# Kernel tuning notes

Hardware: AMD Instinct MI355X
Metric: run time of the kernel (lower is better)

Reference implementation:

```python
import jax, jax.numpy as jnp
import numpy as np

E, TWO_I, H = 8, 3072, 2048
I = TWO_I // 2
T = 16384

def setup_inputs() -> dict:
    key = jax.random.key(0)
    k1, k2, k3 = jax.random.split(key, 3)
    scale_gu = 1.0 / np.sqrt(H)
    scale_dn = 1.0 / np.sqrt(I)
    return {
        "current_state": jax.random.normal(k1, (T, H), dtype=jnp.float32),
        "gate_up_proj": jax.random.normal(k2, (E, TWO_I, H), dtype=jnp.float32) * scale_gu,
        "down_proj": jax.random.normal(k3, (E, H, I), dtype=jnp.float32) * scale_dn,
        "expert_idx": 3,
    }

def reference(current_state, gate_up_proj, down_proj, expert_idx):
    # F.linear(x, W) == x @ W.T
    w_gu = gate_up_proj[expert_idx]            # [2I, H]
    w_dn = down_proj[expert_idx]               # [H, I]
    gu = jnp.einsum("th,ih->ti", current_state, w_gu)  # [T, 2I]
    gate, up = jnp.split(gu, 2, axis=-1)       # each [T, I]
    hidden = jax.nn.silu(gate) * up            # SwiGLU gating
    return jnp.einsum("ti,hi->th", hidden, w_dn)  # [T, H]
```

## Files before the change

kernel.cpp:

```cpp
#include <hip/hip_runtime.h>
#include <hip/hip_bf16.h>


namespace {

constexpr int T_ = 16384;
constexpr int H_ = 2048;
constexpr int I_ = 1536;

typedef short short8 __attribute__((ext_vector_type(8)));
typedef float f32x4 __attribute__((ext_vector_type(4)));
typedef unsigned short ushort4v __attribute__((ext_vector_type(4)));

__device__ __forceinline__ unsigned short f2bf(float f) {
    union { float f; unsigned u; } v; v.f = f;
    return (unsigned short)((v.u + 0x7FFFu + ((v.u >> 16) & 1u)) >> 16);
}

typedef __attribute__((address_space(1))) const void gvoid;
typedef __attribute__((address_space(3))) void lvoid;
__device__ __forceinline__ void gload16(const void* g, void* l) {
    __builtin_amdgcn_global_load_lds((gvoid*)g, (lvoid*)l, 16, 0, 0);
}

__global__ void k_cvt(const float* __restrict__ base, const int* __restrict__ eidx,
                      long sliceElems, unsigned short* __restrict__ dst, int n4) {
    const float* src = base + (size_t)(*eidx) * (size_t)sliceElems;
    int i = blockIdx.x * blockDim.x + threadIdx.x;
    const int stride = gridDim.x * blockDim.x;
    for (; i < n4; i += stride) {
        f32x4 v = ((const f32x4*)src)[i];
        ushort4v h = { f2bf(v[0]), f2bf(v[1]), f2bf(v[2]), f2bf(v[3]) };
        ((ushort4v*)dst)[i] = h;
    }
}

__global__ __launch_bounds__(256, 2) void k_gemm1_swiglu(
    const unsigned short* __restrict__ xb, const unsigned short* __restrict__ wgub,
    unsigned short* __restrict__ hidden)
{
    __shared__ unsigned short lds[3 * 128 * 64];
    unsigned short* ldsA  = lds;
    unsigned short* ldsBg = lds + 128 * 64;
    unsigned short* ldsBu = lds + 2 * 128 * 64;

    const int tid  = threadIdx.x;
    const int lane = tid & 63;
    const int wv   = tid >> 6;
    const int wr   = wv >> 1, wc = wv & 1;

    const int nb = (blockIdx.x & 7) * 192 + (blockIdx.x >> 3);
    const int bx = nb % 12, by = nb / 12;
    const int m0 = by * 128;
    const int n0 = bx * 128;

    f32x4 accG[4][4], accU[4][4];
    #pragma unroll
    for (int a = 0; a < 4; ++a)
        #pragma unroll
        for (int b = 0; b < 4; ++b) { accG[a][b] = (f32x4)0.0f; accU[a][b] = (f32x4)0.0f; }

    const int drow = lane >> 3;
    const int dcol = (lane & 7) * 8;
    const int l15 = lane & 15;
    const int l4  = lane >> 4;

    for (int k0 = 0; k0 < H_; k0 += 64) {
        __syncthreads();
        #pragma unroll
        for (int r = 0; r < 4; ++r) {
            const int row  = r * 32 + wv * 8 + drow;
            const int loff = r * 2048 + wv * 512;
            gload16(xb   + (size_t)(m0 + row)      * H_ + k0 + dcol, ldsA  + loff);
            gload16(wgub + (size_t)(n0 + row)      * H_ + k0 + dcol, ldsBg + loff);
            gload16(wgub + (size_t)(I_ + n0 + row) * H_ + k0 + dcol, ldsBu + loff);
        }
        __syncthreads();

        #pragma unroll
        for (int kk = 0; kk < 2; ++kk) {
            short8 af[4], bg[4], bu[4];
            #pragma unroll
            for (int a = 0; a < 4; ++a) {
                const int r = wr * 64 + a * 16 + l15;
                af[a] = *(const short8*)(ldsA + r * 64 + kk * 32 + l4 * 8);
            }
            #pragma unroll
            for (int b = 0; b < 4; ++b) {
                const int r = wc * 64 + b * 16 + l15;
                bg[b] = *(const short8*)(ldsBg + r * 64 + kk * 32 + l4 * 8);
                bu[b] = *(const short8*)(ldsBu + r * 64 + kk * 32 + l4 * 8);
            }
            #pragma unroll
            for (int a = 0; a < 4; ++a)
                #pragma unroll
                for (int b = 0; b < 4; ++b) {
                    accG[a][b] = __builtin_amdgcn_mfma_f32_16x16x32_bf16(af[a], bg[b], accG[a][b], 0, 0, 0);
                    accU[a][b] = __builtin_amdgcn_mfma_f32_16x16x32_bf16(af[a], bu[b], accU[a][b], 0, 0, 0);
                }
        }
    }

    #pragma unroll
    for (int a = 0; a < 4; ++a)
        #pragma unroll
        for (int b = 0; b < 4; ++b)
            #pragma unroll
            for (int j = 0; j < 4; ++j) {
                const int row = m0 + wr * 64 + a * 16 + l4 * 4 + j;
                const int col = n0 + wc * 64 + b * 16 + l15;
                const float g = accG[a][b][j];
                const float u = accU[a][b][j];
                const float s = g / (1.0f + __expf(-g));
                hidden[(size_t)row * I_ + col] = f2bf(s * u);
            }
}

__global__ __launch_bounds__(256, 2) void k_gemm2(
    const unsigned short* __restrict__ hidden, const unsigned short* __restrict__ wdnb,
    float* __restrict__ out)
{
    __shared__ unsigned short lds[2 * 128 * 64];
    unsigned short* ldsA = lds;
    unsigned short* ldsB = lds + 128 * 64;

    const int tid  = threadIdx.x;
    const int lane = tid & 63;
    const int wv   = tid >> 6;
    const int wr   = wv >> 1, wc = wv & 1;

    const int nb = (blockIdx.x & 7) * 256 + (blockIdx.x >> 3);
    const int bx = nb % 16, by = nb / 16;
    const int m0 = by * 128;
    const int n0 = bx * 128;

    f32x4 acc[4][4];
    #pragma unroll
    for (int a = 0; a < 4; ++a)
        #pragma unroll
        for (int b = 0; b < 4; ++b) acc[a][b] = (f32x4)0.0f;

    const int drow = lane >> 3;
    const int dcol = (lane & 7) * 8;
    const int l15 = lane & 15;
    const int l4  = lane >> 4;

    for (int k0 = 0; k0 < I_; k0 += 64) {
        __syncthreads();
        #pragma unroll
        for (int r = 0; r < 4; ++r) {
            const int row  = r * 32 + wv * 8 + drow;
            const int loff = r * 2048 + wv * 512;
            gload16(hidden + (size_t)(m0 + row) * I_ + k0 + dcol, ldsA + loff);
            gload16(wdnb   + (size_t)(n0 + row) * I_ + k0 + dcol, ldsB + loff);
        }
        __syncthreads();

        #pragma unroll
        for (int kk = 0; kk < 2; ++kk) {
            short8 af[4], bw[4];
            #pragma unroll
            for (int a = 0; a < 4; ++a) {
                const int r = wr * 64 + a * 16 + l15;
                af[a] = *(const short8*)(ldsA + r * 64 + kk * 32 + l4 * 8);
            }
            #pragma unroll
            for (int b = 0; b < 4; ++b) {
                const int r = wc * 64 + b * 16 + l15;
                bw[b] = *(const short8*)(ldsB + r * 64 + kk * 32 + l4 * 8);
            }
            #pragma unroll
            for (int a = 0; a < 4; ++a)
                #pragma unroll
                for (int b = 0; b < 4; ++b)
                    acc[a][b] = __builtin_amdgcn_mfma_f32_16x16x32_bf16(af[a], bw[b], acc[a][b], 0, 0, 0);
        }
    }

    #pragma unroll
    for (int a = 0; a < 4; ++a)
        #pragma unroll
        for (int b = 0; b < 4; ++b)
            #pragma unroll
            for (int j = 0; j < 4; ++j) {
                const int row = m0 + wr * 64 + a * 16 + l4 * 4 + j;
                const int col = n0 + wc * 64 + b * 16 + l15;
                out[(size_t)row * H_ + col] = acc[a][b][j];
            }
}

}

extern "C" void kernel_launch(void* const* d_in, const int* in_sizes, int n_in,
                              void* d_out, int out_size, void* d_ws, size_t ws_size,
                              hipStream_t stream) {
    const float* x   = (const float*)d_in[0];
    const float* wgu = (const float*)d_in[1];
    const float* wdn = (const float*)d_in[2];
    const int* eidx  = (const int*)d_in[3];
    float* out = (float*)d_out;

    unsigned short* xb     = (unsigned short*)d_out;
    unsigned short* hidden = (unsigned short*)d_ws;
    unsigned short* wgub   = (unsigned short*)((char*)d_ws + 50331648);
    unsigned short* wdnb   = (unsigned short*)((char*)d_ws + 62914560);

    k_cvt<<<2048, 256, 0, stream>>>(x, eidx, 0L, xb, (T_ * H_) / 4);
    k_cvt<<<2048, 256, 0, stream>>>(wgu, eidx, (long)(2 * I_) * H_, wgub, (2 * I_ * H_) / 4);
    k_cvt<<<2048, 256, 0, stream>>>(wdn, eidx, (long)H_ * I_, wdnb, (H_ * I_) / 4);
    k_gemm1_swiglu<<<dim3((I_ / 128) * (T_ / 128)), 256, 0, stream>>>(xb, wgub, hidden);
    k_gemm2<<<dim3((H_ / 128) * (T_ / 128)), 256, 0, stream>>>(hidden, wdnb, out);
}
```

Before: 381.8 us.

## Rewrite both GEMMs with 256x256 tiles, 8 waves, 4-stage pipelined global-to-LDS loads

Both GEMM kernels now use 512-thread blocks with 256x256 output tiles (gemm1 packs 128 gate plus 128 up columns), BK=32 and a 4-buffer LDS ring that prefetches two k-steps ahead. Loads are interleaved with MFMA bursts, controlled by explicit vmcnt waits, barriers and setprio. The aim is to hide global latency and raise arithmetic intensity per block. In exchange, gemm1 exchanges the up accumulators through LDS for the SwiGLU epilogue, which leaves half the waves idle there, and the kernels use 128 KB of LDS with heavier register pressure.

```diff
diff --git a/kernel.cpp b/kernel.cpp
--- a/kernel.cpp
+++ b/kernel.cpp
@@ -22,6 +22,10 @@
 __device__ __forceinline__ void gload16(const void* g, void* l) {
     __builtin_amdgcn_global_load_lds((gvoid*)g, (lvoid*)l, 16, 0, 0);
 }
+
+#define SBAR() do { __builtin_amdgcn_s_barrier(); __builtin_amdgcn_sched_barrier(0); } while (0)
+#define VMCNT4() do { asm volatile("s_waitcnt vmcnt(4)" ::: "memory"); __builtin_amdgcn_sched_barrier(0); } while (0)
+#define VMCNT0() do { asm volatile("s_waitcnt vmcnt(0)" ::: "memory"); __builtin_amdgcn_sched_barrier(0); } while (0)
 
 __global__ void k_cvt(const float* __restrict__ base, const int* __restrict__ eidx,
                       long sliceElems, unsigned short* __restrict__ dst, int n4) {
@@ -35,157 +39,256 @@
     }
 }
 
-__global__ __launch_bounds__(256, 2) void k_gemm1_swiglu(
+__global__ __launch_bounds__(512, 2) void k_gemm1_swiglu(
     const unsigned short* __restrict__ xb, const unsigned short* __restrict__ wgub,
     unsigned short* __restrict__ hidden)
 {
-    __shared__ unsigned short lds[3 * 128 * 64];
-    unsigned short* ldsA  = lds;
-    unsigned short* ldsBg = lds + 128 * 64;
-    unsigned short* ldsBu = lds + 2 * 128 * 64;
+    __shared__ unsigned short lds[4 * 16384];
 
     const int tid  = threadIdx.x;
     const int lane = tid & 63;
-    const int wv   = tid >> 6;
-    const int wr   = wv >> 1, wc = wv & 1;
-
-    const int nb = (blockIdx.x & 7) * 192 + (blockIdx.x >> 3);
+    const int wid  = tid >> 6;
+    const int wr   = wid >> 2;
+    const int wc   = wid & 3;
+    const int l15  = lane & 15;
+    const int l4   = lane >> 4;
+
+    const int nb = (blockIdx.x & 7) * 96 + (blockIdx.x >> 3);
     const int bx = nb % 12, by = nb / 12;
-    const int m0 = by * 128;
+    const int m0 = by * 256;
     const int n0 = bx * 128;
 
-    f32x4 accG[4][4], accU[4][4];
-    #pragma unroll
-    for (int a = 0; a < 4; ++a)
-        #pragma unroll
-        for (int b = 0; b < 4; ++b) { accG[a][b] = (f32x4)0.0f; accU[a][b] = (f32x4)0.0f; }
-
-    const int drow = lane >> 3;
-    const int dcol = (lane & 7) * 8;
-    const int l15 = lane & 15;
-    const int l4  = lane >> 4;
-
-    for (int k0 = 0; k0 < H_; k0 += 64) {
-        __syncthreads();
-        #pragma unroll
-        for (int r = 0; r < 4; ++r) {
-            const int row  = r * 32 + wv * 8 + drow;
-            const int loff = r * 2048 + wv * 512;
-            gload16(xb   + (size_t)(m0 + row)      * H_ + k0 + dcol, ldsA  + loff);
-            gload16(wgub + (size_t)(n0 + row)      * H_ + k0 + dcol, ldsBg + loff);
-            gload16(wgub + (size_t)(I_ + n0 + row) * H_ + k0 + dcol, ldsBu + loff);
-        }
-        __syncthreads();
-
-        #pragma unroll
-        for (int kk = 0; kk < 2; ++kk) {
-            short8 af[4], bg[4], bu[4];
-            #pragma unroll
-            for (int a = 0; a < 4; ++a) {
-                const int r = wr * 64 + a * 16 + l15;
-                af[a] = *(const short8*)(ldsA + r * 64 + kk * 32 + l4 * 8);
-            }
-            #pragma unroll
-            for (int b = 0; b < 4; ++b) {
-                const int r = wc * 64 + b * 16 + l15;
-                bg[b] = *(const short8*)(ldsBg + r * 64 + kk * 32 + l4 * 8);
-                bu[b] = *(const short8*)(ldsBu + r * 64 + kk * 32 + l4 * 8);
-            }
-            #pragma unroll
-            for (int a = 0; a < 4; ++a)
+    const int srow = lane >> 2;
+    const int scol = (lane & 3) * 8;
+
+    f32x4 acc[8][4];
+    #pragma unroll
+    for (int m = 0; m < 8; ++m)
+        #pragma unroll
+        for (int n = 0; n < 4; ++n) acc[m][n] = (f32x4)0.0f;
+
+    constexpr int NT = H_ / 32;
+
+    #pragma unroll
+    for (int tt = 0; tt < 2; ++tt) {
+        unsigned short* stA = lds + tt * 16384;
+        unsigned short* stB = stA + 8192;
+        const int kS = tt * 32;
+        #pragma unroll
+        for (int j = 0; j < 2; ++j) {
+            const int rb = (wid * 2 + j) * 16;
+            gload16(xb + (size_t)(m0 + rb + srow) * H_ + kS + scol, stA + rb * 32);
+        }
+        #pragma unroll
+        for (int j = 0; j < 2; ++j) {
+            const int rb = (wid * 2 + j) * 16;
+            const int growb = (rb < 128) ? (n0 + rb) : (I_ + n0 + rb - 128);
+            gload16(wgub + (size_t)(growb + srow) * H_ + kS + scol, stB + rb * 32);
+        }
+    }
+    VMCNT4();
+    SBAR();
+
+    const int aoff = wr * 4096 + l15 * 32 + l4 * 8;
+    const int boff = wc * 2048 + l15 * 32 + l4 * 8;
+
+    for (int t = 0; t < NT; ++t) {
+        const unsigned short* bA = lds + (t & 3) * 16384;
+        const unsigned short* bB = bA + 8192;
+        unsigned short* stA = lds + ((t + 2) & 3) * 16384;
+        unsigned short* stB = stA + 8192;
+        const int kS = (t + 2) * 32;
+        const bool st = (t + 2 < NT);
+
+        short8 bf[4], af[4];
+        #pragma unroll
+        for (int n = 0; n < 4; ++n) bf[n] = *(const short8*)(bB + boff + n * 512);
+        #pragma unroll
+        for (int a = 0; a < 4; ++a) af[a] = *(const short8*)(bA + aoff + a * 512);
+        if (st) {
+            #pragma unroll
+            for (int j = 0; j < 2; ++j) {
+                const int rb = (wid * 2 + j) * 16;
+                gload16(xb + (size_t)(m0 + rb + srow) * H_ + kS + scol, stA + rb * 32);
+            }
+        }
+        SBAR();
+        __builtin_amdgcn_s_setprio(1);
+        #pragma unroll
+        for (int a = 0; a < 4; ++a)
+            #pragma unroll
+            for (int n = 0; n < 4; ++n)
+                acc[a][n] = __builtin_amdgcn_mfma_f32_16x16x32_bf16(af[a], bf[n], acc[a][n], 0, 0, 0);
+        __builtin_amdgcn_s_setprio(0);
+        SBAR();
+
+        #pragma unroll
+        for (int a = 0; a < 4; ++a) af[a] = *(const short8*)(bA + aoff + 2048 + a * 512);
+        if (st) {
+            #pragma unroll
+            for (int j = 0; j < 2; ++j) {
+                const int rb = (wid * 2 + j) * 16;
+                const int growb = (rb < 128) ? (n0 + rb) : (I_ + n0 + rb - 128);
+                gload16(wgub + (size_t)(growb + srow) * H_ + kS + scol, stB + rb * 32);
+            }
+        }
+        SBAR();
+        __builtin_amdgcn_s_setprio(1);
+        #pragma unroll
+        for (int a = 0; a < 4; ++a)
+            #pragma unroll
+            for (int n = 0; n < 4; ++n)
+                acc[4 + a][n] = __builtin_amdgcn_mfma_f32_16x16x32_bf16(af[a], bf[n], acc[4 + a][n], 0, 0, 0);
+        __builtin_amdgcn_s_setprio(0);
+        if (t < NT - 2)       { VMCNT4(); }
+        else if (t == NT - 2) { VMCNT0(); }
+        SBAR();
+    }
+
+    float* exch = (float*)lds;
+    if (wc >= 2) {
+        #pragma unroll
+        for (int m = 0; m < 8; ++m)
+            #pragma unroll
+            for (int n = 0; n < 4; ++n)
                 #pragma unroll
-                for (int b = 0; b < 4; ++b) {
-                    accG[a][b] = __builtin_amdgcn_mfma_f32_16x16x32_bf16(af[a], bg[b], accG[a][b], 0, 0, 0);
-                    accU[a][b] = __builtin_amdgcn_mfma_f32_16x16x32_bf16(af[a], bu[b], accU[a][b], 0, 0, 0);
+                for (int j = 0; j < 4; ++j) {
+                    const int row = wr * 128 + m * 16 + l4 * 4 + j;
+                    const int col = (wc - 2) * 64 + n * 16 + l15;
+                    exch[row * 128 + col] = acc[m][n][j];
                 }
-        }
-    }
-
-    #pragma unroll
-    for (int a = 0; a < 4; ++a)
-        #pragma unroll
-        for (int b = 0; b < 4; ++b)
-            #pragma unroll
-            for (int j = 0; j < 4; ++j) {
-                const int row = m0 + wr * 64 + a * 16 + l4 * 4 + j;
-                const int col = n0 + wc * 64 + b * 16 + l15;
-                const float g = accG[a][b][j];
-                const float u = accU[a][b][j];
-                const float s = g / (1.0f + __expf(-g));
-                hidden[(size_t)row * I_ + col] = f2bf(s * u);
-            }
-}
-
-__global__ __launch_bounds__(256, 2) void k_gemm2(
+    }
+    __syncthreads();
+    if (wc < 2) {
+        #pragma unroll
+        for (int m = 0; m < 8; ++m)
+            #pragma unroll
+            for (int n = 0; n < 4; ++n)
+                #pragma unroll
+                for (int j = 0; j < 4; ++j) {
+                    const int row = wr * 128 + m * 16 + l4 * 4 + j;
+                    const int col = wc * 64 + n * 16 + l15;
+                    const float g = acc[m][n][j];
+                    const float u = exch[row * 128 + col];
+                    const float s = g / (1.0f + __expf(-g));
+                    hidden[(size_t)(m0 + row) * I_ + n0 + col] = f2bf(s * u);
+                }
+    }
+}
+
+__global__ __launch_bounds__(512, 2) void k_gemm2(
     const unsigned short* __restrict__ hidden, const unsigned short* __restrict__ wdnb,
     float* __restrict__ out)
 {
-    __shared__ unsigned short lds[2 * 128 * 64];
-    unsigned short* ldsA = lds;
-    unsigned short* ldsB = lds + 128 * 64;
+    __shared__ unsigned short lds[4 * 16384];
 
     const int tid  = threadIdx.x;
     const int lane = tid & 63;
-    const int wv   = tid >> 6;
-    const int wr   = wv >> 1, wc = wv & 1;
-
-    const int nb = (blockIdx.x & 7) * 256 + (blockIdx.x >> 3);
-    const int bx = nb % 16, by = nb / 16;
-    const int m0 = by * 128;
-    const int n0 = bx * 128;
-
-    f32x4 acc[4][4];
-    #pragma unroll
-    for (int a = 0; a < 4; ++a)
-        #pragma unroll
-        for (int b = 0; b < 4; ++b) acc[a][b] = (f32x4)0.0f;
-
-    const int drow = lane >> 3;
-    const int dcol = (lane & 7) * 8;
-    const int l15 = lane & 15;
-    const int l4  = lane >> 4;
-
-    for (int k0 = 0; k0 < I_; k0 += 64) {
-        __syncthreads();
-        #pragma unroll
-        for (int r = 0; r < 4; ++r) {
-            const int row  = r * 32 + wv * 8 + drow;
-            const int loff = r * 2048 + wv * 512;
-            gload16(hidden + (size_t)(m0 + row) * I_ + k0 + dcol, ldsA + loff);
-            gload16(wdnb   + (size_t)(n0 + row) * I_ + k0 + dcol, ldsB + loff);
-        }
-        __syncthreads();
-
-        #pragma unroll
-        for (int kk = 0; kk < 2; ++kk) {
-            short8 af[4], bw[4];
-            #pragma unroll
-            for (int a = 0; a < 4; ++a) {
-                const int r = wr * 64 + a * 16 + l15;
-                af[a] = *(const short8*)(ldsA + r * 64 + kk * 32 + l4 * 8);
-            }
-            #pragma unroll
-            for (int b = 0; b < 4; ++b) {
-                const int r = wc * 64 + b * 16 + l15;
-                bw[b] = *(const short8*)(ldsB + r * 64 + kk * 32 + l4 * 8);
-            }
-            #pragma unroll
-            for (int a = 0; a < 4; ++a)
-                #pragma unroll
-                for (int b = 0; b < 4; ++b)
-                    acc[a][b] = __builtin_amdgcn_mfma_f32_16x16x32_bf16(af[a], bw[b], acc[a][b], 0, 0, 0);
-        }
-    }
-
-    #pragma unroll
-    for (int a = 0; a < 4; ++a)
-        #pragma unroll
-        for (int b = 0; b < 4; ++b)
+    const int wid  = tid >> 6;
+    const int wr   = wid >> 2;
+    const int wc   = wid & 3;
+    const int l15  = lane & 15;
+    const int l4   = lane >> 4;
+
+    const int nb = (blockIdx.x & 7) * 64 + (blockIdx.x >> 3);
+    const int bx = nb & 7, by = nb >> 3;
+    const int m0 = by * 256;
+    const int n0 = bx * 256;
+
+    const int srow = lane >> 2;
+    const int scol = (lane & 3) * 8;
+
+    f32x4 acc[8][4];
+    #pragma unroll
+    for (int m = 0; m < 8; ++m)
+        #pragma unroll
+        for (int n = 0; n < 4; ++n) acc[m][n] = (f32x4)0.0f;
+
+    constexpr int NT = I_ / 32;
+
+    #pragma unroll
+    for (int tt = 0; tt < 2; ++tt) {
+        unsigned short* stA = lds + tt * 16384;
+        unsigned short* stB = stA + 8192;
+        const int kS = tt * 32;
+        #pragma unroll
+        for (int j = 0; j < 2; ++j) {
+            const int rb = (wid * 2 + j) * 16;
+            gload16(hidden + (size_t)(m0 + rb + srow) * I_ + kS + scol, stA + rb * 32);
+        }
+        #pragma unroll
+        for (int j = 0; j < 2; ++j) {
+            const int rb = (wid * 2 + j) * 16;
+            gload16(wdnb + (size_t)(n0 + rb + srow) * I_ + kS + scol, stB + rb * 32);
+        }
+    }
+    VMCNT4();
+    SBAR();
+
+    const int aoff = wr * 4096 + l15 * 32 + l4 * 8;
+    const int boff = wc * 2048 + l15 * 32 + l4 * 8;
+
+    for (int t = 0; t < NT; ++t) {
+        const unsigned short* bA = lds + (t & 3) * 16384;
+        const unsigned short* bB = bA + 8192;
+        unsigned short* stA = lds + ((t + 2) & 3) * 16384;
+        unsigned short* stB = stA + 8192;
+        const int kS = (t + 2) * 32;
+        const bool st = (t + 2 < NT);
+
+        short8 bf[4], af[4];
+        #pragma unroll
+        for (int n = 0; n < 4; ++n) bf[n] = *(const short8*)(bB + boff + n * 512);
+        #pragma unroll
+        for (int a = 0; a < 4; ++a) af[a] = *(const short8*)(bA + aoff + a * 512);
+        if (st) {
+            #pragma unroll
+            for (int j = 0; j < 2; ++j) {
+                const int rb = (wid * 2 + j) * 16;
+                gload16(hidden + (size_t)(m0 + rb + srow) * I_ + kS + scol, stA + rb * 32);
+            }
+        }
+        SBAR();
+        __builtin_amdgcn_s_setprio(1);
+        #pragma unroll
+        for (int a = 0; a < 4; ++a)
+            #pragma unroll
+            for (int n = 0; n < 4; ++n)
+                acc[a][n] = __builtin_amdgcn_mfma_f32_16x16x32_bf16(af[a], bf[n], acc[a][n], 0, 0, 0);
+        __builtin_amdgcn_s_setprio(0);
+        SBAR();
+
+        #pragma unroll
+        for (int a = 0; a < 4; ++a) af[a] = *(const short8*)(bA + aoff + 2048 + a * 512);
+        if (st) {
+            #pragma unroll
+            for (int j = 0; j < 2; ++j) {
+                const int rb = (wid * 2 + j) * 16;
+                gload16(wdnb + (size_t)(n0 + rb + srow) * I_ + kS + scol, stB + rb * 32);
+            }
+        }
+        SBAR();
+        __builtin_amdgcn_s_setprio(1);
+        #pragma unroll
+        for (int a = 0; a < 4; ++a)
+            #pragma unroll
+            for (int n = 0; n < 4; ++n)
+                acc[4 + a][n] = __builtin_amdgcn_mfma_f32_16x16x32_bf16(af[a], bf[n], acc[4 + a][n], 0, 0, 0);
+        __builtin_amdgcn_s_setprio(0);
+        if (t < NT - 2)       { VMCNT4(); }
+        else if (t == NT - 2) { VMCNT0(); }
+        SBAR();
+    }
+
+    #pragma unroll
+    for (int m = 0; m < 8; ++m)
+        #pragma unroll
+        for (int n = 0; n < 4; ++n)
             #pragma unroll
             for (int j = 0; j < 4; ++j) {
-                const int row = m0 + wr * 64 + a * 16 + l4 * 4 + j;
-                const int col = n0 + wc * 64 + b * 16 + l15;
-                out[(size_t)row * H_ + col] = acc[a][b][j];
+                const int row = m0 + wr * 128 + m * 16 + l4 * 4 + j;
+                const int col = n0 + wc * 64 + n * 16 + l15;
+                out[(size_t)row * H_ + col] = acc[m][n][j];
             }
 }
 
@@ -208,6 +311,6 @@
     k_cvt<<<2048, 256, 0, stream>>>(x, eidx, 0L, xb, (T_ * H_) / 4);
     k_cvt<<<2048, 256, 0, stream>>>(wgu, eidx, (long)(2 * I_) * H_, wgub, (2 * I_ * H_) / 4);
     k_cvt<<<2048, 256, 0, stream>>>(wdn, eidx, (long)H_ * I_, wdnb, (H_ * I_) / 4);
-    k_gemm1_swiglu<<<dim3((I_ / 128) * (T_ / 128)), 256, 0, stream>>>(xb, wgub, hidden);
-    k_gemm2<<<dim3((H_ / 128) * (T_ / 128)), 256, 0, stream>>>(hidden, wdnb, out);
-}
+    k_gemm1_swiglu<<<dim3((T_ / 256) * (I_ / 128)), 512, 0, stream>>>(xb, wgub, hidden);
+    k_gemm2<<<dim3((T_ / 256) * (H_ / 256)), 512, 0, stream>>>(hidden, wdnb, out);
+}
```

Result: no change. 382.4 us (+0.1%).
